# Performance work log

Hardware: AMD Instinct MI355X
Metric: run time of the kernel (lower is better)

Reference implementation:

```python
import jax, jax.numpy as jnp
import numpy as np

FH, FW = 4, 4  # patch/filter spatial size (non-overlapping tiles)

def _to_patches(X, fh, fw):
    # X: (N, H, W, C) -> (N, P, fh, fw, C), P = (H//fh)*(W//fw)
    N, H, W, C = X.shape
    nr, nc = H // fh, W // fw
    x = X.reshape(N, nr, fh, nc, fw, C).transpose(0, 1, 3, 2, 4, 5)
    return x.reshape(N, nr * nc, fh, fw, C)

def setup_inputs() -> dict:
    key = jax.random.key(0)
    k1, k2 = jax.random.split(key)
    N, H, W, FIN, FOUT = 32, 128, 128, 32, 32
    P = (H // FH) * (W // FW)
    X = jax.random.normal(k1, (N, H, W, FIN), dtype=jnp.float32)
    filters = jax.random.normal(k2, (P, FH, FW, FIN, FOUT), dtype=jnp.float32) * 0.01  # 'alexnet' init
    bias = jnp.zeros((FOUT,), dtype=jnp.float32)
    return {"X": X, "filters": filters, "bias": bias}

def reference(X, filters, bias):
    N, H, W, C = X.shape
    nr, nc = H // FH, W // FW
    patches = _to_patches(X, FH, FW)                       # (N, P, fh, fw, fin)
    # locally-connected conv: unique filter per patch location (batched GEMM over p)
    Z = jnp.einsum('npijc,pijco->npo', patches, filters)   # (N, P, fout)
    Z = Z + bias
    A = jax.nn.relu(Z)
    return A.reshape(N, nr, nc, -1)                        # (N, H/fh, W/fw, fout)
```

## Files before the change

### kernel.cpp

```cpp
#include <hip/hip_runtime.h>


typedef __attribute__((ext_vector_type(4))) float f32x4;
typedef __attribute__((ext_vector_type(4))) short s16x4;
typedef __attribute__((ext_vector_type(8))) short s16x8;

#define HWC   (128 * 128 * 32)
#define WC    (128 * 32)
#define KTOT  512
#define FOUT  32
#define XROW  516
#define FROW  260

__device__ __forceinline__ short f2bf(float f) {
    unsigned u = __builtin_bit_cast(unsigned, f);
    u += 0x7fffu + ((u >> 16) & 1u);
    return (short)(u >> 16);
}

__launch_bounds__(256)
__global__ void lcconv_kernel(const float* __restrict__ X,
                              const float* __restrict__ F,
                              const float* __restrict__ bias,
                              float* __restrict__ out) {
    __shared__ short Xs[32 * XROW];
    __shared__ short Fs[32 * FROW];

    const int p    = blockIdx.x;
    const int pr   = p >> 5;
    const int pc   = p & 31;
    const int tid  = threadIdx.x;
    const int lane = tid & 63;
    const int w    = tid >> 6;
    const int mi   = (w >> 1) * 16;
    const int ni   = (w & 1) * 16;

    {
        const int xbase = pr * 4 * WC + pc * (4 * 32);
        #pragma unroll 4
        for (int it = 0; it < 16; ++it) {
            int idx = it * 256 + tid;
            int n   = idx >> 7;
            int r   = idx & 127;
            int i   = r >> 5;
            int w4  = r & 31;
            const float* gp = X + n * HWC + xbase + i * WC + w4 * 4;
            f32x4 v = *(const f32x4*)gp;
            s16x4 b;
            b[0] = f2bf(v[0]); b[1] = f2bf(v[1]); b[2] = f2bf(v[2]); b[3] = f2bf(v[3]);
            int k = i * 128 + w4 * 4;
            *(s16x4*)(&Xs[n * XROW + k]) = b;
        }
    }

    f32x4 acc = {0.f, 0.f, 0.f, 0.f};
    const int arow = mi + (lane & 15);
    const int brow = ni + (lane & 15);
    const int g16  = (lane >> 4) * 8;

    const float* Fp = F + p * (KTOT * FOUT);

    #pragma unroll
    for (int h = 0; h < 2; ++h) {
        #pragma unroll
        for (int it = 0; it < 2; ++it) {
            int task = it * 256 + tid;
            int o4   = task & 7;
            int k4   = task >> 3;
            const float* fp0 = Fp + (h * 256 + k4 * 4) * FOUT + o4 * 4;
            f32x4 d0 = *(const f32x4*)(fp0 + 0 * FOUT);
            f32x4 d1 = *(const f32x4*)(fp0 + 1 * FOUT);
            f32x4 d2 = *(const f32x4*)(fp0 + 2 * FOUT);
            f32x4 d3 = *(const f32x4*)(fp0 + 3 * FOUT);
            #pragma unroll
            for (int e = 0; e < 4; ++e) {
                s16x4 b;
                b[0] = f2bf(d0[e]); b[1] = f2bf(d1[e]);
                b[2] = f2bf(d2[e]); b[3] = f2bf(d3[e]);
                *(s16x4*)(&Fs[(o4 * 4 + e) * FROW + k4 * 4]) = b;
            }
        }
        __syncthreads();

        #pragma unroll
        for (int ks = 0; ks < 8; ++ks) {
            const short* ap = &Xs[arow * XROW + h * 256 + ks * 32 + g16];
            const short* bp = &Fs[brow * FROW + ks * 32 + g16];
            s16x4 alo = *(const s16x4*)(ap);
            s16x4 ahi = *(const s16x4*)(ap + 4);
            s16x4 blo = *(const s16x4*)(bp);
            s16x4 bhi = *(const s16x4*)(bp + 4);
            s16x8 a, b;
            a[0] = alo[0]; a[1] = alo[1]; a[2] = alo[2]; a[3] = alo[3];
            a[4] = ahi[0]; a[5] = ahi[1]; a[6] = ahi[2]; a[7] = ahi[3];
            b[0] = blo[0]; b[1] = blo[1]; b[2] = blo[2]; b[3] = blo[3];
            b[4] = bhi[0]; b[5] = bhi[1]; b[6] = bhi[2]; b[7] = bhi[3];
            acc = __builtin_amdgcn_mfma_f32_16x16x32_bf16(a, b, acc, 0, 0, 0);
        }
        __syncthreads();
    }

    const int o_g = ni + (lane & 15);
    const float bv = bias[o_g];
    #pragma unroll
    for (int r = 0; r < 4; ++r) {
        int n_g = mi + (lane >> 4) * 4 + r;
        float v = acc[r] + bv;
        v = v > 0.f ? v : 0.f;
        out[n_g * (1024 * FOUT) + p * FOUT + o_g] = v;
    }
}

extern "C" void kernel_launch(void* const* d_in, const int* in_sizes, int n_in,
                              void* d_out, int out_size, void* d_ws, size_t ws_size,
                              hipStream_t stream) {
    const float* X    = (const float*)d_in[0];
    const float* F    = (const float*)d_in[1];
    const float* bias = (const float*)d_in[2];
    float* out        = (float*)d_out;
    lcconv_kernel<<<dim3(1024), dim3(256), 0, stream>>>(X, F, bias, out);
}
```

Before: 147.4 us.

## Split X staging into K halves and prefetch second half during first MFMA pass

```diff
diff --git a/kernel.cpp b/kernel.cpp
--- a/kernel.cpp
+++ b/kernel.cpp
@@ -5,12 +5,10 @@
 typedef __attribute__((ext_vector_type(4))) short s16x4;
 typedef __attribute__((ext_vector_type(8))) short s16x8;
 
-#define HWC   (128 * 128 * 32)
-#define WC    (128 * 32)
-#define KTOT  512
-#define FOUT  32
-#define XROW  516
-#define FROW  260
+#define HWC (128 * 128 * 32)
+#define WC  (128 * 32)
+#define FOUT 32
+#define ROW 264
 
 __device__ __forceinline__ short f2bf(float f) {
     unsigned u = __builtin_bit_cast(unsigned, f);
@@ -18,13 +16,19 @@
     return (short)(u >> 16);
 }
 
-__launch_bounds__(256)
+__device__ __forceinline__ void barrier_lds_only() {
+    asm volatile("s_waitcnt lgkmcnt(0)" ::: "memory");
+    __builtin_amdgcn_s_barrier();
+    asm volatile("" ::: "memory");
+}
+
+__launch_bounds__(256, 4)
 __global__ void lcconv_kernel(const float* __restrict__ X,
                               const float* __restrict__ F,
                               const float* __restrict__ bias,
                               float* __restrict__ out) {
-    __shared__ short Xs[32 * XROW];
-    __shared__ short Fs[32 * FROW];
+    __shared__ short Xs[32 * ROW];
+    __shared__ short Fs[32 * ROW];
 
     const int p    = blockIdx.x;
     const int pr   = p >> 5;
@@ -35,70 +39,90 @@
     const int mi   = (w >> 1) * 16;
     const int ni   = (w & 1) * 16;
 
-    {
-        const int xbase = pr * 4 * WC + pc * (4 * 32);
-        #pragma unroll 4
-        for (int it = 0; it < 16; ++it) {
+    const int xbase = pr * 4 * WC + pc * 128;
+    const float* Fp = F + p * (512 * FOUT);
+
+    auto loadX = [&](f32x4* xv, int h) {
+        #pragma unroll
+        for (int it = 0; it < 8; ++it) {
             int idx = it * 256 + tid;
-            int n   = idx >> 7;
-            int r   = idx & 127;
-            int i   = r >> 5;
-            int w4  = r & 31;
-            const float* gp = X + n * HWC + xbase + i * WC + w4 * 4;
-            f32x4 v = *(const f32x4*)gp;
+            int n   = idx >> 6;
+            int il  = (idx >> 5) & 1;
+            int w4  = idx & 31;
+            xv[it] = *(const f32x4*)(X + n * HWC + xbase + (2 * h + il) * WC + w4 * 4);
+        }
+    };
+    auto loadF = [&](f32x4* fv, int h) {
+        #pragma unroll
+        for (int tt = 0; tt < 2; ++tt) {
+            int task = tt * 256 + tid;
+            int o4   = task & 7;
+            int k4   = task >> 3;
+            const float* fp0 = Fp + (h * 256 + k4 * 4) * FOUT + o4 * 4;
+            #pragma unroll
+            for (int d = 0; d < 4; ++d)
+                fv[tt * 4 + d] = *(const f32x4*)(fp0 + d * FOUT);
+        }
+    };
+    auto storeLDS = [&](const f32x4* xv, const f32x4* fv) {
+        #pragma unroll
+        for (int it = 0; it < 8; ++it) {
+            int idx = it * 256 + tid;
+            int n   = idx >> 6;
+            int il  = (idx >> 5) & 1;
+            int w4  = idx & 31;
             s16x4 b;
-            b[0] = f2bf(v[0]); b[1] = f2bf(v[1]); b[2] = f2bf(v[2]); b[3] = f2bf(v[3]);
-            int k = i * 128 + w4 * 4;
-            *(s16x4*)(&Xs[n * XROW + k]) = b;
+            b[0] = f2bf(xv[it][0]); b[1] = f2bf(xv[it][1]);
+            b[2] = f2bf(xv[it][2]); b[3] = f2bf(xv[it][3]);
+            *(s16x4*)(&Xs[n * ROW + il * 128 + w4 * 4]) = b;
         }
-    }
+        #pragma unroll
+        for (int tt = 0; tt < 2; ++tt) {
+            int task = tt * 256 + tid;
+            int o4   = task & 7;
+            int k4   = task >> 3;
+            #pragma unroll
+            for (int e = 0; e < 4; ++e) {
+                s16x4 b;
+                b[0] = f2bf(fv[tt * 4 + 0][e]); b[1] = f2bf(fv[tt * 4 + 1][e]);
+                b[2] = f2bf(fv[tt * 4 + 2][e]); b[3] = f2bf(fv[tt * 4 + 3][e]);
+                *(s16x4*)(&Fs[(o4 * 4 + e) * ROW + k4 * 4]) = b;
+            }
+        }
+    };
 
-    f32x4 acc = {0.f, 0.f, 0.f, 0.f};
     const int arow = mi + (lane & 15);
     const int brow = ni + (lane & 15);
     const int g16  = (lane >> 4) * 8;
 
-    const float* Fp = F + p * (KTOT * FOUT);
-
-    #pragma unroll
-    for (int h = 0; h < 2; ++h) {
-        #pragma unroll
-        for (int it = 0; it < 2; ++it) {
-            int task = it * 256 + tid;
-            int o4   = task & 7;
-            int k4   = task >> 3;
-            const float* fp0 = Fp + (h * 256 + k4 * 4) * FOUT + o4 * 4;
-            f32x4 d0 = *(const f32x4*)(fp0 + 0 * FOUT);
-            f32x4 d1 = *(const f32x4*)(fp0 + 1 * FOUT);
-            f32x4 d2 = *(const f32x4*)(fp0 + 2 * FOUT);
-            f32x4 d3 = *(const f32x4*)(fp0 + 3 * FOUT);
-            #pragma unroll
-            for (int e = 0; e < 4; ++e) {
-                s16x4 b;
-                b[0] = f2bf(d0[e]); b[1] = f2bf(d1[e]);
-                b[2] = f2bf(d2[e]); b[3] = f2bf(d3[e]);
-                *(s16x4*)(&Fs[(o4 * 4 + e) * FROW + k4 * 4]) = b;
-            }
-        }
-        __syncthreads();
-
+    f32x4 acc = {0.f, 0.f, 0.f, 0.f};
+    auto mfmaHalf = [&]() {
         #pragma unroll
         for (int ks = 0; ks < 8; ++ks) {
-            const short* ap = &Xs[arow * XROW + h * 256 + ks * 32 + g16];
-            const short* bp = &Fs[brow * FROW + ks * 32 + g16];
-            s16x4 alo = *(const s16x4*)(ap);
-            s16x4 ahi = *(const s16x4*)(ap + 4);
-            s16x4 blo = *(const s16x4*)(bp);
-            s16x4 bhi = *(const s16x4*)(bp + 4);
-            s16x8 a, b;
-            a[0] = alo[0]; a[1] = alo[1]; a[2] = alo[2]; a[3] = alo[3];
-            a[4] = ahi[0]; a[5] = ahi[1]; a[6] = ahi[2]; a[7] = ahi[3];
-            b[0] = blo[0]; b[1] = blo[1]; b[2] = blo[2]; b[3] = blo[3];
-            b[4] = bhi[0]; b[5] = bhi[1]; b[6] = bhi[2]; b[7] = bhi[3];
+            s16x8 a = *(const s16x8*)(&Xs[arow * ROW + ks * 32 + g16]);
+            s16x8 b = *(const s16x8*)(&Fs[brow * ROW + ks * 32 + g16]);
             acc = __builtin_amdgcn_mfma_f32_16x16x32_bf16(a, b, acc, 0, 0, 0);
         }
-        __syncthreads();
-    }
+    };
+
+    f32x4 xa[8], fa[8], xb[8], fb[8];
+
+    loadX(xa, 0);
+    loadF(fa, 0);
+    storeLDS(xa, fa);
+    loadX(xb, 1);
+    loadF(fb, 1);
+    barrier_lds_only();
+
+    mfmaHalf();
+
+    __builtin_amdgcn_s_barrier();
+    asm volatile("" ::: "memory");
+
+    storeLDS(xb, fb);
+    barrier_lds_only();
+
+    mfmaHalf();
 
     const int o_g = ni + (lane & 15);
     const float bv = bias[o_g];
```

Result: no change. 148.1 us (+0.5%).

## Load MFMA operands directly from global memory with split-K across waves

Applied to the files above, without the earlier changes.

```diff
diff --git a/kernel.cpp b/kernel.cpp
--- a/kernel.cpp
+++ b/kernel.cpp
@@ -2,29 +2,35 @@
 
 
 typedef __attribute__((ext_vector_type(4))) float f32x4;
-typedef __attribute__((ext_vector_type(4))) short s16x4;
 typedef __attribute__((ext_vector_type(8))) short s16x8;
 
-#define HWC   (128 * 128 * 32)
-#define WC    (128 * 32)
-#define KTOT  512
-#define FOUT  32
-#define XROW  516
-#define FROW  260
+#define HWC (128 * 128 * 32)
+#define WC  (128 * 32)
 
 __device__ __forceinline__ short f2bf(float f) {
     unsigned u = __builtin_bit_cast(unsigned, f);
     u += 0x7fffu + ((u >> 16) & 1u);
     return (short)(u >> 16);
 }
+__device__ __forceinline__ s16x8 pack8(const f32x4 lo, const f32x4 hi) {
+    s16x8 r;
+    r[0] = f2bf(lo[0]); r[1] = f2bf(lo[1]); r[2] = f2bf(lo[2]); r[3] = f2bf(lo[3]);
+    r[4] = f2bf(hi[0]); r[5] = f2bf(hi[1]); r[6] = f2bf(hi[2]); r[7] = f2bf(hi[3]);
+    return r;
+}
+__device__ __forceinline__ s16x8 pack8f(const float* b) {
+    s16x8 r;
+    #pragma unroll
+    for (int j = 0; j < 8; ++j) r[j] = f2bf(b[j]);
+    return r;
+}
 
-__launch_bounds__(256)
+__launch_bounds__(256, 4)
 __global__ void lcconv_kernel(const float* __restrict__ X,
                               const float* __restrict__ F,
                               const float* __restrict__ bias,
                               float* __restrict__ out) {
-    __shared__ short Xs[32 * XROW];
-    __shared__ short Fs[32 * FROW];
+    __shared__ f32x4 red[4][4][64];
 
     const int p    = blockIdx.x;
     const int pr   = p >> 5;
@@ -32,82 +38,74 @@
     const int tid  = threadIdx.x;
     const int lane = tid & 63;
     const int w    = tid >> 6;
-    const int mi   = (w >> 1) * 16;
-    const int ni   = (w & 1) * 16;
+    const int col  = lane & 15;
+    const int g    = lane >> 4;
 
-    {
-        const int xbase = pr * 4 * WC + pc * (4 * 32);
-        #pragma unroll 4
-        for (int it = 0; it < 16; ++it) {
-            int idx = it * 256 + tid;
-            int n   = idx >> 7;
-            int r   = idx & 127;
-            int i   = r >> 5;
-            int w4  = r & 31;
-            const float* gp = X + n * HWC + xbase + i * WC + w4 * 4;
-            f32x4 v = *(const f32x4*)gp;
-            s16x4 b;
-            b[0] = f2bf(v[0]); b[1] = f2bf(v[1]); b[2] = f2bf(v[2]); b[3] = f2bf(v[3]);
-            int k = i * 128 + w4 * 4;
-            *(s16x4*)(&Xs[n * XROW + k]) = b;
+    const float* A0p = X + col * HWC + (pr * 4 + w) * WC + pc * 128 + g * 8;
+    const float* A1p = A0p + 16 * HWC;
+    const float* Bp  = F + p * (512 * 32) + (w * 128 + g * 8) * 32 + col;
+
+    f32x4 aA[2][2], aB[2][2];
+    float bA[2][8], bB[2][8];
+
+    auto load = [&](int ks, f32x4 (&a)[2][2], float (&b)[2][8]) {
+        const float* a0 = A0p + ks * 32;
+        const float* a1 = A1p + ks * 32;
+        a[0][0] = *(const f32x4*)(a0);  a[0][1] = *(const f32x4*)(a0 + 4);
+        a[1][0] = *(const f32x4*)(a1);  a[1][1] = *(const f32x4*)(a1 + 4);
+        const float* bp = Bp + ks * 1024;
+        #pragma unroll
+        for (int j = 0; j < 8; ++j) {
+            b[0][j] = bp[j * 32];
+            b[1][j] = bp[j * 32 + 16];
         }
-    }
+    };
 
-    f32x4 acc = {0.f, 0.f, 0.f, 0.f};
-    const int arow = mi + (lane & 15);
-    const int brow = ni + (lane & 15);
-    const int g16  = (lane >> 4) * 8;
+    f32x4 acc00{0,0,0,0}, acc01{0,0,0,0}, acc10{0,0,0,0}, acc11{0,0,0,0};
+    auto compute = [&](const f32x4 (&a)[2][2], const float (&b)[2][8]) {
+        s16x8 A0 = pack8(a[0][0], a[0][1]);
+        s16x8 A1 = pack8(a[1][0], a[1][1]);
+        s16x8 B0 = pack8f(b[0]);
+        s16x8 B1 = pack8f(b[1]);
+        acc00 = __builtin_amdgcn_mfma_f32_16x16x32_bf16(A0, B0, acc00, 0, 0, 0);
+        acc01 = __builtin_amdgcn_mfma_f32_16x16x32_bf16(A0, B1, acc01, 0, 0, 0);
+        acc10 = __builtin_amdgcn_mfma_f32_16x16x32_bf16(A1, B0, acc10, 0, 0, 0);
+        acc11 = __builtin_amdgcn_mfma_f32_16x16x32_bf16(A1, B1, acc11, 0, 0, 0);
+    };
 
-    const float* Fp = F + p * (KTOT * FOUT);
+    load(0, aA, bA);
+    load(1, aB, bB);
+    __builtin_amdgcn_sched_barrier(0);
+    compute(aA, bA);
+    load(2, aA, bA);
+    __builtin_amdgcn_sched_barrier(0);
+    compute(aB, bB);
+    load(3, aB, bB);
+    __builtin_amdgcn_sched_barrier(0);
+    compute(aA, bA);
+    compute(aB, bB);
 
-    #pragma unroll
-    for (int h = 0; h < 2; ++h) {
-        #pragma unroll
-        for (int it = 0; it < 2; ++it) {
-            int task = it * 256 + tid;
-            int o4   = task & 7;
-            int k4   = task >> 3;
-            const float* fp0 = Fp + (h * 256 + k4 * 4) * FOUT + o4 * 4;
-            f32x4 d0 = *(const f32x4*)(fp0 + 0 * FOUT);
-            f32x4 d1 = *(const f32x4*)(fp0 + 1 * FOUT);
-            f32x4 d2 = *(const f32x4*)(fp0 + 2 * FOUT);
-            f32x4 d3 = *(const f32x4*)(fp0 + 3 * FOUT);
-            #pragma unroll
-            for (int e = 0; e < 4; ++e) {
-                s16x4 b;
-                b[0] = f2bf(d0[e]); b[1] = f2bf(d1[e]);
-                b[2] = f2bf(d2[e]); b[3] = f2bf(d3[e]);
-                *(s16x4*)(&Fs[(o4 * 4 + e) * FROW + k4 * 4]) = b;
-            }
-        }
-        __syncthreads();
+    red[w][0][lane] = acc00;
+    red[w][1][lane] = acc01;
+    red[w][2][lane] = acc10;
+    red[w][3][lane] = acc11;
+    __syncthreads();
 
-        #pragma unroll
-        for (int ks = 0; ks < 8; ++ks) {
-            const short* ap = &Xs[arow * XROW + h * 256 + ks * 32 + g16];
-            const short* bp = &Fs[brow * FROW + ks * 32 + g16];
-            s16x4 alo = *(const s16x4*)(ap);
-            s16x4 ahi = *(const s16x4*)(ap + 4);
-            s16x4 blo = *(const s16x4*)(bp);
-            s16x4 bhi = *(const s16x4*)(bp + 4);
-            s16x8 a, b;
-            a[0] = alo[0]; a[1] = alo[1]; a[2] = alo[2]; a[3] = alo[3];
-            a[4] = ahi[0]; a[5] = ahi[1]; a[6] = ahi[2]; a[7] = ahi[3];
-            b[0] = blo[0]; b[1] = blo[1]; b[2] = blo[2]; b[3] = blo[3];
-            b[4] = bhi[0]; b[5] = bhi[1]; b[6] = bhi[2]; b[7] = bhi[3];
-            acc = __builtin_amdgcn_mfma_f32_16x16x32_bf16(a, b, acc, 0, 0, 0);
-        }
-        __syncthreads();
-    }
+    const int nh = w >> 1, oh = w & 1;
+    f32x4 s  = red[0][w][lane];
+    f32x4 t1 = red[1][w][lane];
+    f32x4 t2 = red[2][w][lane];
+    f32x4 t3 = red[3][w][lane];
+    s += t1; s += t2; s += t3;
 
-    const int o_g = ni + (lane & 15);
+    const int o_g = oh * 16 + col;
     const float bv = bias[o_g];
     #pragma unroll
     for (int r = 0; r < 4; ++r) {
-        int n_g = mi + (lane >> 4) * 4 + r;
-        float v = acc[r] + bv;
+        int n_g = nh * 16 + g * 4 + r;
+        float v = s[r] + bv;
         v = v > 0.f ? v : 0.f;
-        out[n_g * (1024 * FOUT) + p * FOUT + o_g] = v;
+        out[n_g * (1024 * 32) + p * 32 + o_g] = v;
     }
 }
 
```

After: 147.8 us. Within noise of the previous version (+0.3%).
